# Kernel optimization log

Hardware: AMD Instinct MI355X
Metric: run time of the kernel (lower is better)

## Reference

```python
import jax, jax.numpy as jnp
import numpy as np

NUM_NODES = 100000
NUM_EDGES = 1600000


def gcn_conv(x, row, col, W, b, num_nodes):
    # PyG GCNConv: out = D^{-1/2} (A + I) D^{-1/2} X W + b
    loop = jnp.arange(num_nodes)
    row = jnp.concatenate([row, loop])
    col = jnp.concatenate([col, loop])
    h = x @ W  # [N, out_dim]
    deg = jax.ops.segment_sum(jnp.ones_like(col, dtype=h.dtype), col,
                              num_segments=num_nodes)
    dinv = jnp.where(deg > 0, jax.lax.rsqrt(deg), 0.0)
    norm = dinv[row] * dinv[col]  # [E+N]
    msg = norm[:, None] * h[row]  # gather + scale
    out = jax.ops.segment_sum(msg, col, num_segments=num_nodes)  # scatter-add
    return out + b


def setup_inputs() -> dict:
    key = jax.random.key(0)
    k1, k2, k3, k4 = jax.random.split(key, 4)
    x = jax.random.normal(k1, (NUM_NODES, 16), dtype=jnp.float32)
    edge_index = jax.random.randint(k2, (2, NUM_EDGES), 0, NUM_NODES, dtype=jnp.int64)
    W1 = jax.random.normal(k3, (16, 32), dtype=jnp.float32) * (1.0 / np.sqrt(16))
    b1 = jnp.zeros((32,), dtype=jnp.float32)
    W2 = jax.random.normal(k4, (32, 16), dtype=jnp.float32) * (1.0 / np.sqrt(32))
    b2 = jnp.zeros((16,), dtype=jnp.float32)
    return {"x": x, "edge_index": edge_index, "W1": W1, "b1": b1, "W2": W2, "b2": b2}


def reference(x, edge_index, W1, b1, W2, b2):
    row, col = edge_index[0], edge_index[1]
    h = gcn_conv(x, row, col, W1, b1, NUM_NODES)
    h = jax.nn.relu(h)
    out = gcn_conv(h, row, col, W2, b2, NUM_NODES)
    return out
```

## Files before the change

### kernel.cpp

```cpp
#include <hip/hip_runtime.h>
#include <hip/hip_fp16.h>

#define NB 196
#define NPB 512
#define BCAP 40
#define REGION 10240
#define ECAP1 4224
#define ECAP2 2560

__global__ __launch_bounds__(512) void k_bucket(
    const int* __restrict__ row, const int* __restrict__ col,
    unsigned* __restrict__ gbuf, int* __restrict__ gtail, int E) {
    __shared__ unsigned sbuf[NB][BCAP];
    __shared__ int scnt[NB];
    __shared__ int gbase[NB];
    const int tid = threadIdx.x;
    int beg = blockIdx.x * 4096;
    int end = beg + 4096; if (end > E) end = E;
    if (tid < NB) scnt[tid] = 0;
    __syncthreads();
    int base = beg + tid * 8;
    if (base < end) {
        int r[8], c[8];
        if (base + 8 <= end) {
            const int4* rp = (const int4*)(row + base);
            const int4* cp = (const int4*)(col + base);
            int4 a = rp[0], b = rp[1], d = cp[0], e = cp[1];
            r[0]=a.x; r[1]=a.y; r[2]=a.z; r[3]=a.w; r[4]=b.x; r[5]=b.y; r[6]=b.z; r[7]=b.w;
            c[0]=d.x; c[1]=d.y; c[2]=d.z; c[3]=d.w; c[4]=e.x; c[5]=e.y; c[6]=e.z; c[7]=e.w;
        } else {
            for (int j = 0; j < 8; ++j) {
                int e2 = base + j;
                r[j] = (e2 < end) ? row[e2] : -1;
                c[j] = (e2 < end) ? col[e2] : -1;
            }
        }
#pragma unroll
        for (int j = 0; j < 8; ++j) {
            if (c[j] < 0) continue;
            int b_ = c[j] >> 9;
            unsigned pk = ((unsigned)r[j] << 9) | (unsigned)(c[j] & 511);
            int p = atomicAdd(&scnt[b_], 1);
            if (p < BCAP) sbuf[b_][p] = pk;
            else {
                int g = atomicAdd(&gtail[b_], 1);
                if (g < REGION) gbuf[(size_t)b_ * REGION + g] = pk;
            }
        }
    }
    __syncthreads();
    if (tid < NB) {
        int n = scnt[tid]; if (n > BCAP) n = BCAP;
        gbase[tid] = (n > 0) ? atomicAdd(&gtail[tid], n) : 0;
    }
    __syncthreads();
    for (int t = tid; t < NB * 4; t += 512) {
        int b_ = t >> 2, part = t & 3;
        int n = scnt[b_]; if (n > BCAP) n = BCAP;
        if (n <= 0) continue;
        int g0 = gbase[b_];
        int lo = (n * part) >> 2;
        int hi = (n * (part + 1)) >> 2;
        for (int i = lo; i < hi; ++i) {
            int g = g0 + i;
            if (g < REGION) gbuf[(size_t)b_ * REGION + g] = sbuf[b_][i];
        }
    }
}

__global__ void k_build(const unsigned* __restrict__ gbuf, const int* __restrict__ gtail,
                        const float* __restrict__ x,
                        int* __restrict__ offs, float* __restrict__ dinv,
                        int* __restrict__ erow, __half* __restrict__ xs, int N) {
    __shared__ int s[256];
    __shared__ int hist[NPB];
    __shared__ int pos[NPB];
    __shared__ int psum[256];
    __shared__ int erow_l[REGION];
    __shared__ int eb_s;
    int b = blockIdx.x;
    int tid = threadIdx.x;
    int v = 0;
    if (tid < NB) { v = gtail[tid]; if (v > REGION) v = REGION; }
    s[tid] = v;
    __syncthreads();
    for (int d = 1; d < 256; d <<= 1) {
        int t = (tid >= d) ? s[tid - d] : 0;
        __syncthreads();
        s[tid] += t;
        __syncthreads();
    }
    if (tid == b) eb_s = s[tid] - v;
    if (b == 0 && tid == NB - 1) offs[N] = s[tid];
    __syncthreads();
    int eb = eb_s;
    int nloc = gtail[b]; if (nloc > REGION) nloc = REGION;
    const unsigned* ebuf = gbuf + (size_t)b * REGION;
    hist[tid] = 0; hist[tid + 256] = 0;
    __syncthreads();
    for (int i = tid; i < nloc; i += 256) atomicAdd(&hist[ebuf[i] & 511u], 1);
    __syncthreads();
    int h0 = hist[2*tid], h1 = hist[2*tid+1];
    psum[tid] = h0 + h1;
    __syncthreads();
    for (int d = 1; d < 256; d <<= 1) {
        int t = (tid >= d) ? psum[tid - d] : 0;
        __syncthreads();
        psum[tid] += t;
        __syncthreads();
    }
    int basep = (tid > 0) ? psum[tid - 1] : 0;
    int e0 = basep, e1 = e0 + h0;
    pos[2*tid] = e0; pos[2*tid+1] = e1;
    int gn = b * NPB + 2 * tid;
    float di0 = rsqrtf((float)h0 + 1.0f);
    float di1 = rsqrtf((float)h1 + 1.0f);
    if (gn   < N) { offs[gn]   = eb + e0; dinv[gn]   = di0; }
    if (gn+1 < N) { offs[gn+1] = eb + e1; dinv[gn+1] = di1; }
    __syncthreads();
    for (int i = tid; i < nloc; i += 256) {
        unsigned pk = ebuf[i];
        int p = atomicAdd(&pos[pk & 511u], 1);
        erow_l[p] = (int)(pk >> 9);
    }
    __syncthreads();
    for (int i = tid; i < nloc; i += 256) erow[eb + i] = erow_l[i];
#pragma unroll
    for (int w = 0; w < 2; ++w) {
        int n = gn + w;
        if (n < N) {
            float di = w ? di1 : di0;
            const float4* xp = (const float4*)(x + (size_t)n * 16);
            float4 v0 = xp[0], v1 = xp[1], v2 = xp[2], v3 = xp[3];
            float4 st[2]; __half2* pp = (__half2*)st;
            pp[0] = __floats2half2_rn(di * v0.x, di * v0.y);
            pp[1] = __floats2half2_rn(di * v0.z, di * v0.w);
            pp[2] = __floats2half2_rn(di * v1.x, di * v1.y);
            pp[3] = __floats2half2_rn(di * v1.z, di * v1.w);
            pp[4] = __floats2half2_rn(di * v2.x, di * v2.y);
            pp[5] = __floats2half2_rn(di * v2.z, di * v2.w);
            pp[6] = __floats2half2_rn(di * v3.x, di * v3.y);
            pp[7] = __floats2half2_rn(di * v3.z, di * v3.w);
            float4* dst = (float4*)(xs + (size_t)n * 16);
            dst[0] = st[0]; dst[1] = st[1];
        }
    }
}

__device__ inline void acc8(float4 v, float* s) {
    const __half2* hp = (const __half2*)&v;
#pragma unroll
    for (int k = 0; k < 4; ++k) {
        float2 f = __half22float2(hp[k]);
        s[2*k]   += f.x;
        s[2*k+1] += f.y;
    }
}

__global__ void k_agg1(const int* __restrict__ offs, const int* __restrict__ erow,
                       const __half* __restrict__ xs, const float* __restrict__ dinv,
                       const float* __restrict__ W1, const float* __restrict__ b1,
                       const float* __restrict__ W2, __half* __restrict__ h2s, int N) {
    __shared__ int offL[129];
    __shared__ float w1s[512];
    __shared__ float w2s[512];
    __shared__ float b1s[32];
    __shared__ float hv[128][17];
    __shared__ __align__(16) char ubuf[16896];
    int* eL = (int*)ubuf;
    float (*hh)[33] = (float(*)[33])ubuf;
    int tid = threadIdx.x;
    for (int t = tid; t < 512; t += 256) { w1s[t] = W1[t]; w2s[t] = W2[t]; }
    if (tid < 32) b1s[tid] = b1[tid];
    int n0 = blockIdx.x * 128;
    int nn = N - n0; if (nn > 128) nn = 128;
    for (int i = tid; i <= nn; i += 256) offL[i] = offs[n0 + i];
    __syncthreads();
    int base = offL[0];
    int cnt = offL[nn] - base; if (cnt > ECAP1) cnt = ECAP1;
    for (int i = tid; i < cnt; i += 256) eL[i] = erow[base + i];
    __syncthreads();
    int m = tid >> 1;
    int q = tid & 1;
    int n = n0 + m;
    float di = 0.0f;
    if (m < nn) {
        float s[8] = {0,0,0,0,0,0,0,0};
        di = dinv[n];
        const __half* hq = xs + q * 8;
        acc8(*(const float4*)(hq + (size_t)n * 16), s);
        int e0 = offL[m], e1 = offL[m + 1];
        int elim = base + ECAP1; if (elim > e1) elim = e1;
        int e = e0;
        for (; e + 3 < elim; e += 4) {
            int r0 = eL[e - base], r1 = eL[e + 1 - base];
            int r2 = eL[e + 2 - base], r3 = eL[e + 3 - base];
            float4 v0 = *(const float4*)(hq + (size_t)r0 * 16);
            float4 v1 = *(const float4*)(hq + (size_t)r1 * 16);
            float4 v2 = *(const float4*)(hq + (size_t)r2 * 16);
            float4 v3 = *(const float4*)(hq + (size_t)r3 * 16);
            acc8(v0, s); acc8(v1, s); acc8(v2, s); acc8(v3, s);
        }
        for (; e < elim; ++e) {
            int r = eL[e - base];
            acc8(*(const float4*)(hq + (size_t)r * 16), s);
        }
        for (; e < e1; ++e) {
            int r = erow[e];
            acc8(*(const float4*)(hq + (size_t)r * 16), s);
        }
#pragma unroll
        for (int j = 0; j < 8; ++j) hv[m][q * 8 + j] = di * s[j];
    }
    __syncthreads();
    if (m < nn) {
        int k0 = q * 16;
        float hid[16];
#pragma unroll
        for (int k = 0; k < 16; ++k) hid[k] = b1s[k0 + k];
#pragma unroll
        for (int c = 0; c < 16; ++c) {
            float a = hv[m][c];
#pragma unroll
            for (int k = 0; k < 16; ++k)
                hid[k] = fmaf(a, w1s[c * 32 + k0 + k], hid[k]);
        }
#pragma unroll
        for (int k = 0; k < 16; ++k) hh[m][k0 + k] = fmaxf(hid[k], 0.0f);
    }
    __syncthreads();
    if (m < nn) {
        int j0 = q * 8;
        float o[8] = {0,0,0,0,0,0,0,0};
#pragma unroll
        for (int k = 0; k < 32; ++k) {
            float a = hh[m][k];
#pragma unroll
            for (int j = 0; j < 8; ++j)
                o[j] = fmaf(a, w2s[k * 16 + j0 + j], o[j]);
        }
        float4 st;
        __half2* pp = (__half2*)&st;
#pragma unroll
        for (int p = 0; p < 4; ++p)
            pp[p] = __floats2half2_rn(di * o[2*p], di * o[2*p+1]);
        *(float4*)(h2s + (size_t)n * 16 + j0) = st;
    }
}

__global__ void k_agg2(const int* __restrict__ offs, const int* __restrict__ erow,
                       const __half* __restrict__ h, const float* __restrict__ dinv,
                       const float* __restrict__ b2, float* __restrict__ out, int N) {
    __shared__ int offL[129];
    __shared__ int eL[ECAP2];
    int tid = threadIdx.x;
    int n0 = blockIdx.x * 128;
    int nn = N - n0; if (nn > 128) nn = 128;
    for (int i = tid; i <= nn; i += 256) offL[i] = offs[n0 + i];
    __syncthreads();
    int base = offL[0];
    int cnt = offL[nn] - base; if (cnt > ECAP2) cnt = ECAP2;
    for (int i = tid; i < cnt; i += 256) eL[i] = erow[base + i];
    __syncthreads();
    int m = tid >> 1;
    int q = tid & 1;
    int n = n0 + m;
    if (m >= nn) return;
    float s[8] = {0,0,0,0,0,0,0,0};
    const __half* hq = h + q * 8;
    acc8(*(const float4*)(hq + (size_t)n * 16), s);
    int e0 = offL[m], e1 = offL[m + 1];
    int elim = base + ECAP2; if (elim > e1) elim = e1;
    int e = e0;
    for (; e + 3 < elim; e += 4) {
        int r0 = eL[e - base], r1 = eL[e + 1 - base];
        int r2 = eL[e + 2 - base], r3 = eL[e + 3 - base];
        float4 v0 = *(const float4*)(hq + (size_t)r0 * 16);
        float4 v1 = *(const float4*)(hq + (size_t)r1 * 16);
        float4 v2 = *(const float4*)(hq + (size_t)r2 * 16);
        float4 v3 = *(const float4*)(hq + (size_t)r3 * 16);
        acc8(v0, s); acc8(v1, s); acc8(v2, s); acc8(v3, s);
    }
    for (; e < elim; ++e) {
        int r = eL[e - base];
        acc8(*(const float4*)(hq + (size_t)r * 16), s);
    }
    for (; e < e1; ++e) {
        int r = erow[e];
        acc8(*(const float4*)(hq + (size_t)r * 16), s);
    }
    float di = dinv[n];
    float4 ba = *(const float4*)(b2 + q * 8);
    float4 bb = *(const float4*)(b2 + q * 8 + 4);
    float4* op = (float4*)(out + (size_t)n * 16 + q * 8);
    op[0] = make_float4(fmaf(di, s[0], ba.x), fmaf(di, s[1], ba.y),
                        fmaf(di, s[2], ba.z), fmaf(di, s[3], ba.w));
    op[1] = make_float4(fmaf(di, s[4], bb.x), fmaf(di, s[5], bb.y),
                        fmaf(di, s[6], bb.z), fmaf(di, s[7], bb.w));
}

extern "C" void kernel_launch(void* const* d_in, const int* in_sizes, int n_in,
                              void* d_out, int out_size, void* d_ws, size_t ws_size,
                              hipStream_t stream) {
    const float* x  = (const float*)d_in[0];
    const int*   ei = (const int*)d_in[1];
    const float* W1 = (const float*)d_in[2];
    const float* b1 = (const float*)d_in[3];
    const float* W2 = (const float*)d_in[4];
    const float* b2 = (const float*)d_in[5];
    float* out = (float*)d_out;

    const int N = in_sizes[0] / 16;
    const int E = in_sizes[1] / 2;
    const int* row = ei;
    const int* col = ei + E;

    float* ws   = (float*)d_ws;
    float* dinv = ws;
    __half* xs  = (__half*)(dinv + N);
    __half* h2s = xs + (size_t)N * 16;
    int* offs  = (int*)(h2s + (size_t)N * 16);
    int* erow  = offs + N + 1;
    int* gtail = erow + E;
    unsigned* gbuf = (unsigned*)(gtail + NB);

    const int nbB = (E + 4095) / 4096;

    hipMemsetAsync(gtail, 0, NB * sizeof(int), stream);
    k_bucket<<<nbB, 512, 0, stream>>>(row, col, gbuf, gtail, E);
    k_build<<<NB, 256, 0, stream>>>(gbuf, gtail, x, offs, dinv, erow, xs, N);
    k_agg1<<<(N + 127) / 128, 256, 0, stream>>>(offs, erow, xs, dinv, W1, b1, W2, h2s, N);
    k_agg2<<<(N + 127) / 128, 256, 0, stream>>>(offs, erow, h2s, dinv, b2, out, N);
}
```

Before: 87.11 us.

## Replace global atomic bucket tails with count pass and per-block prefix offsets

Adds a counting kernel that records per-block bucket counts into a transposed table. The bucketing kernel then derives deterministic write offsets from prefix sums of that table instead of doing global atomicAdd on bucket tails, and the memset is dropped. This removes global atomic contention and makes the bucket layout deterministic. In exchange, col is read a second time in an extra kernel launch, and each block runs a serial prefix loop over up to 391 entries.

```diff
diff --git a/kernel.cpp b/kernel.cpp
--- a/kernel.cpp
+++ b/kernel.cpp
@@ -4,21 +4,58 @@
 #define NB 196
 #define NPB 512
 #define BCAP 40
+#define NBLKP 392
 #define REGION 10240
 #define ECAP1 4224
 #define ECAP2 2560
 
+__global__ __launch_bounds__(512) void k_count(
+    const int* __restrict__ col, int* __restrict__ cntT, int E) {
+    __shared__ int scnt[NB];
+    const int blk = blockIdx.x, tid = threadIdx.x;
+    if (tid < NB) scnt[tid] = 0;
+    __syncthreads();
+    int beg = blk * 4096;
+    int end = beg + 4096; if (end > E) end = E;
+    int base = beg + tid * 8;
+    if (base < end) {
+        int c[8];
+        if (base + 8 <= end) {
+            const int4* cp = (const int4*)(col + base);
+            int4 d = cp[0], e = cp[1];
+            c[0]=d.x; c[1]=d.y; c[2]=d.z; c[3]=d.w; c[4]=e.x; c[5]=e.y; c[6]=e.z; c[7]=e.w;
+        } else {
+            for (int j = 0; j < 8; ++j) {
+                int e2 = base + j;
+                c[j] = (e2 < end) ? col[e2] : -1;
+            }
+        }
+#pragma unroll
+        for (int j = 0; j < 8; ++j)
+            if (c[j] >= 0) atomicAdd(&scnt[c[j] >> 9], 1);
+    }
+    __syncthreads();
+    if (tid < NB) cntT[tid * NBLKP + blk] = scnt[tid];
+}
+
 __global__ __launch_bounds__(512) void k_bucket(
     const int* __restrict__ row, const int* __restrict__ col,
-    unsigned* __restrict__ gbuf, int* __restrict__ gtail, int E) {
+    const int* __restrict__ cntT, unsigned* __restrict__ gbuf, int E) {
     __shared__ unsigned sbuf[NB][BCAP];
     __shared__ int scnt[NB];
-    __shared__ int gbase[NB];
-    const int tid = threadIdx.x;
-    int beg = blockIdx.x * 4096;
+    __shared__ int basL[NB];
+    const int blk = blockIdx.x, tid = threadIdx.x;
+    if (tid < NB) {
+        const int* cr = cntT + tid * NBLKP;
+        int s = 0;
+#pragma unroll 4
+        for (int i = 0; i < blk; ++i) s += cr[i];
+        basL[tid] = s;
+        scnt[tid] = 0;
+    }
+    __syncthreads();
+    int beg = blk * 4096;
     int end = beg + 4096; if (end > E) end = E;
-    if (tid < NB) scnt[tid] = 0;
-    __syncthreads();
     int base = beg + tid * 8;
     if (base < end) {
         int r[8], c[8];
@@ -43,22 +80,17 @@
             int p = atomicAdd(&scnt[b_], 1);
             if (p < BCAP) sbuf[b_][p] = pk;
             else {
-                int g = atomicAdd(&gtail[b_], 1);
+                int g = basL[b_] + p;
                 if (g < REGION) gbuf[(size_t)b_ * REGION + g] = pk;
             }
         }
-    }
-    __syncthreads();
-    if (tid < NB) {
-        int n = scnt[tid]; if (n > BCAP) n = BCAP;
-        gbase[tid] = (n > 0) ? atomicAdd(&gtail[tid], n) : 0;
     }
     __syncthreads();
     for (int t = tid; t < NB * 4; t += 512) {
         int b_ = t >> 2, part = t & 3;
         int n = scnt[b_]; if (n > BCAP) n = BCAP;
         if (n <= 0) continue;
-        int g0 = gbase[b_];
+        int g0 = basL[b_];
         int lo = (n * part) >> 2;
         int hi = (n * (part + 1)) >> 2;
         for (int i = lo; i < hi; ++i) {
@@ -68,11 +100,13 @@
     }
 }
 
-__global__ void k_build(const unsigned* __restrict__ gbuf, const int* __restrict__ gtail,
+__global__ void k_build(const unsigned* __restrict__ gbuf, const int* __restrict__ cntT,
                         const float* __restrict__ x,
                         int* __restrict__ offs, float* __restrict__ dinv,
-                        int* __restrict__ erow, __half* __restrict__ xs, int N) {
+                        int* __restrict__ erow, __half* __restrict__ xs,
+                        int N, int nblk) {
     __shared__ int s[256];
+    __shared__ int Tb[256];
     __shared__ int hist[NPB];
     __shared__ int pos[NPB];
     __shared__ int psum[256];
@@ -81,7 +115,13 @@
     int b = blockIdx.x;
     int tid = threadIdx.x;
     int v = 0;
-    if (tid < NB) { v = gtail[tid]; if (v > REGION) v = REGION; }
+    if (tid < NB) {
+        const int* cr = cntT + tid * NBLKP;
+#pragma unroll 4
+        for (int i = 0; i < nblk; ++i) v += cr[i];
+        if (v > REGION) v = REGION;
+    }
+    Tb[tid] = v;
     s[tid] = v;
     __syncthreads();
     for (int d = 1; d < 256; d <<= 1) {
@@ -94,7 +134,7 @@
     if (b == 0 && tid == NB - 1) offs[N] = s[tid];
     __syncthreads();
     int eb = eb_s;
-    int nloc = gtail[b]; if (nloc > REGION) nloc = REGION;
+    int nloc = Tb[b];
     const unsigned* ebuf = gbuf + (size_t)b * REGION;
     hist[tid] = 0; hist[tid + 256] = 0;
     __syncthreads();
@@ -177,8 +217,8 @@
     for (int i = tid; i <= nn; i += 256) offL[i] = offs[n0 + i];
     __syncthreads();
     int base = offL[0];
-    int cnt = offL[nn] - base; if (cnt > ECAP1) cnt = ECAP1;
-    for (int i = tid; i < cnt; i += 256) eL[i] = erow[base + i];
+    int cnt_ = offL[nn] - base; if (cnt_ > ECAP1) cnt_ = ECAP1;
+    for (int i = tid; i < cnt_; i += 256) eL[i] = erow[base + i];
     __syncthreads();
     int m = tid >> 1;
     int q = tid & 1;
@@ -259,8 +299,8 @@
     for (int i = tid; i <= nn; i += 256) offL[i] = offs[n0 + i];
     __syncthreads();
     int base = offL[0];
-    int cnt = offL[nn] - base; if (cnt > ECAP2) cnt = ECAP2;
-    for (int i = tid; i < cnt; i += 256) eL[i] = erow[base + i];
+    int cnt_ = offL[nn] - base; if (cnt_ > ECAP2) cnt_ = ECAP2;
+    for (int i = tid; i < cnt_; i += 256) eL[i] = erow[base + i];
     __syncthreads();
     int m = tid >> 1;
     int q = tid & 1;
@@ -314,6 +354,7 @@
     const int E = in_sizes[1] / 2;
     const int* row = ei;
     const int* col = ei + E;
+    const int nblk = (E + 4095) / 4096;
 
     float* ws   = (float*)d_ws;
     float* dinv = ws;
@@ -321,14 +362,12 @@
     __half* h2s = xs + (size_t)N * 16;
     int* offs  = (int*)(h2s + (size_t)N * 16);
     int* erow  = offs + N + 1;
-    int* gtail = erow + E;
-    unsigned* gbuf = (unsigned*)(gtail + NB);
-
-    const int nbB = (E + 4095) / 4096;
-
-    hipMemsetAsync(gtail, 0, NB * sizeof(int), stream);
-    k_bucket<<<nbB, 512, 0, stream>>>(row, col, gbuf, gtail, E);
-    k_build<<<NB, 256, 0, stream>>>(gbuf, gtail, x, offs, dinv, erow, xs, N);
+    int* cntT  = erow + E;
+    unsigned* gbuf = (unsigned*)(cntT + NB * NBLKP);
+
+    k_count<<<nblk, 512, 0, stream>>>(col, cntT, E);
+    k_bucket<<<nblk, 512, 0, stream>>>(row, col, cntT, gbuf, E);
+    k_build<<<NB, 256, 0, stream>>>(gbuf, cntT, x, offs, dinv, erow, xs, N, nblk);
     k_agg1<<<(N + 127) / 128, 256, 0, stream>>>(offs, erow, xs, dinv, W1, b1, W2, h2s, N);
     k_agg2<<<(N + 127) / 128, 256, 0, stream>>>(offs, erow, h2s, dinv, b2, out, N);
 }
```

Result: slower. 97.57 us (+12.0%).
